# Performance work log

Hardware: AMD Instinct MI355X
Metric: run time of the kernel (lower is better)

Reference implementation:

```python
import jax, jax.numpy as jnp
import numpy as np

NEG_SLOPE = 0.01  # nn.LeakyReLU default


def setup_inputs() -> dict:
    key = jax.random.key(0)
    k1, k2, k3, k4, k5 = jax.random.split(key, 5)
    SLI, FEAT, NODE = 8, 64, 20000
    N = SLI * NODE          # 160000 graph nodes
    E = 2_560_000           # avg degree 16
    OUT = 64
    inputs = jax.random.normal(k1, (SLI, FEAT, NODE), dtype=jnp.float32)
    src = jax.random.randint(k2, (E,), 0, N, dtype=jnp.int64)
    dst = jax.random.randint(k3, (E,), 0, N, dtype=jnp.int64)
    # GraphConv params (glorot-ish scale)
    W = jax.random.normal(k4, (FEAT, OUT), dtype=jnp.float32) / np.sqrt(FEAT)
    b = jnp.zeros((OUT,), dtype=jnp.float32)
    return {"inputs": inputs, "W": W, "b": b, "src": src, "dst": dst}


def reference(inputs, W, b, src, dst):
    # inputs: [sli, feat, node] -> [sli*node, feat]  (dropout is eval-mode identity)
    sli, feat, node = inputs.shape
    x = jnp.transpose(inputs, (0, 2, 1)).reshape(-1, feat)
    N = sli * node
    ones = jnp.ones(src.shape, dtype=x.dtype)
    deg_out = jax.ops.segment_sum(ones, src, num_segments=N)  # out-degree of src
    deg_in = jax.ops.segment_sum(ones, dst, num_segments=N)   # in-degree of dst
    norm_src = jnp.where(deg_out > 0, deg_out, 1.0) ** -0.5
    norm_dst = jnp.where(deg_in > 0, deg_in, 1.0) ** -0.5
    # norm='both': scale src feats, sum-aggregate over edges, scale dst
    h = x * norm_src[:, None]
    agg = jax.ops.segment_sum(h[src], dst, num_segments=N)    # [N, feat]
    agg = agg * norm_dst[:, None]
    out = agg @ W + b                                          # [N, out]
    out = jax.nn.leaky_relu(out, NEG_SLOPE)
    # [N, out] -> [sli, node, out] -> [sli, out, node]
    return jnp.transpose(out.reshape(sli, node, -1), (0, 2, 1))
```

## Files before the change

### kernel.cpp

```cpp
#include <hip/hip_runtime.h>
#include <hip/hip_bf16.h>

constexpr int SLI  = 8;
constexpr int FEAT = 64;
constexpr int NODE = 20000;
constexpr int NTOT = SLI * NODE;
constexpr int OUTF = 64;
constexpr int CAP  = 48;
constexpr int NBD  = 625;
constexpr int NBS  = 313;
constexpr int BCAPD = 4864;
constexpr int BCAPS = 8960;
constexpr int EPB  = 4096;
constexpr int NDST = NTOT / 256;

typedef __attribute__((ext_vector_type(8))) short bf16x8;
typedef __attribute__((ext_vector_type(4))) float f32x4;

static __device__ inline unsigned short f2bf(float x) {
    unsigned u = __float_as_uint(x);
    unsigned r = (u + 0x7fffu + ((u >> 16) & 1u)) >> 16;
    return (unsigned short)r;
}

__global__ __launch_bounds__(256) void k_part(const int* __restrict__ src,
                                              const int* __restrict__ dst,
                                              int* __restrict__ cursor_d,
                                              unsigned* __restrict__ bucket_d,
                                              int* __restrict__ cursor_s,
                                              unsigned short* __restrict__ bucket_s, int E) {
    __shared__ unsigned       svalD[EPB];
    __shared__ unsigned short sbktD[EPB];
    __shared__ unsigned sS[EPB];
    __shared__ int histD[NBD], lcurD[NBD], baseD[NBD];
    __shared__ int histS[NBS], lcurS[NBS], baseS[NBS];
    __shared__ int goffD[64], goffS[64];
    int t  = threadIdx.x;
    int e0 = blockIdx.x * EPB;
    for (int i = t; i < NBD; i += 256) histD[i] = 0;
    for (int i = t; i < NBS; i += 256) histS[i] = 0;
    __syncthreads();
    int myS[16], myD[16];
#pragma unroll
    for (int i = 0; i < 4; ++i) {
        int j  = (e0 >> 2) + i * 256 + t;
        int b4 = j << 2;
        if (b4 + 3 < E) {
            int4 vs = ((const int4*)src)[j];
            int4 vd = ((const int4*)dst)[j];
            myS[4*i+0] = vs.x; myS[4*i+1] = vs.y; myS[4*i+2] = vs.z; myS[4*i+3] = vs.w;
            myD[4*i+0] = vd.x; myD[4*i+1] = vd.y; myD[4*i+2] = vd.z; myD[4*i+3] = vd.w;
        } else {
#pragma unroll
            for (int c = 0; c < 4; ++c) {
                int idx = b4 + c;
                myS[4*i+c] = (idx < E) ? src[idx] : -1;
                myD[4*i+c] = (idx < E) ? dst[idx] : -1;
            }
        }
    }
#pragma unroll
    for (int i = 0; i < 16; ++i) {
        if (myD[i] >= 0) {
            atomicAdd(&histD[myD[i] >> 8], 1);
            atomicAdd(&histS[myS[i] >> 9], 1);
        }
    }
    __syncthreads();
    int rbD[3], rbS[2];
#pragma unroll
    for (int i = 0; i < 3; ++i) {
        int bb = t + i * 256;
        rbD[i] = (bb < NBD) ? atomicAdd(&cursor_d[bb], histD[bb]) : 0;
    }
#pragma unroll
    for (int i = 0; i < 2; ++i) {
        int bb = t + i * 256;
        rbS[i] = (bb < NBS) ? atomicAdd(&cursor_s[bb], histS[bb]) : 0;
    }
    int wv = t >> 6, ln = t & 63;
    if (wv == 0) {
        int b0 = ln * 10, s = 0;
#pragma unroll
        for (int j = 0; j < 10; ++j) { int bb = b0 + j; if (bb < NBD) s += histD[bb]; }
        int x = s;
        for (int off = 1; off < 64; off <<= 1) {
            int y = __shfl_up(x, off, 64);
            if (ln >= off) x += y;
        }
        goffD[ln] = x - s;
    } else if (wv == 1) {
        int b0 = ln * 5, s = 0;
#pragma unroll
        for (int j = 0; j < 5; ++j) { int bb = b0 + j; if (bb < NBS) s += histS[bb]; }
        int x = s;
        for (int off = 1; off < 64; off <<= 1) {
            int y = __shfl_up(x, off, 64);
            if (ln >= off) x += y;
        }
        goffS[ln] = x - s;
    }
    asm volatile("s_waitcnt lgkmcnt(0)\n\ts_barrier" ::: "memory");
    for (int bb = t; bb < NBD; bb += 256) {
        int g = bb / 10;
        int sD = goffD[g];
        for (int k = g * 10; k < bb; ++k) sD += histD[k];
        lcurD[bb] = sD;
    }
    for (int bb = t; bb < NBS; bb += 256) {
        int g = bb / 5;
        int sS2 = goffS[g];
        for (int k = g * 5; k < bb; ++k) sS2 += histS[k];
        lcurS[bb] = sS2;
    }
    asm volatile("s_waitcnt lgkmcnt(0)\n\ts_barrier" ::: "memory");
#pragma unroll
    for (int i = 0; i < 16; ++i) {
        if (myD[i] >= 0) {
            int bD = myD[i] >> 8;
            int p  = atomicAdd(&lcurD[bD], 1);
            svalD[p] = ((unsigned)(myD[i] & 255) << 18) | (unsigned)myS[i];
            sbktD[p] = (unsigned short)bD;
            int bS = myS[i] >> 9;
            int q  = atomicAdd(&lcurS[bS], 1);
            sS[q] = ((unsigned)bS << 9) | (unsigned)(myS[i] & 511);
        }
    }
#pragma unroll
    for (int i = 0; i < 3; ++i) { int bb = t + i * 256; if (bb < NBD) baseD[bb] = rbD[i]; }
#pragma unroll
    for (int i = 0; i < 2; ++i) { int bb = t + i * 256; if (bb < NBS) baseS[bb] = rbS[i]; }
    __syncthreads();
    int nval = E - e0; if (nval > EPB) nval = EPB;
    for (int p = t; p < nval; p += 256) {
        int bD = sbktD[p];
        int wi = baseD[bD] + (p - (lcurD[bD] - histD[bD]));
        if (wi < BCAPD) bucket_d[(size_t)bD * BCAPD + wi] = svalD[p];
        unsigned vs = sS[p];
        int bS = vs >> 9;
        int wj = baseS[bS] + (p - (lcurS[bS] - histS[bS]));
        if (wj < BCAPS) bucket_s[(size_t)bS * BCAPS + wj] = (unsigned short)(vs & 511);
    }
}

__global__ __launch_bounds__(512) void k_fin(const int* __restrict__ cursor_d,
                                             const unsigned* __restrict__ bucket_d,
                                             const int* __restrict__ cursor_s,
                                             const unsigned short* __restrict__ bucket_s,
                                             int* __restrict__ col_ell,
                                             int* __restrict__ deg_in,
                                             int* __restrict__ deg_out) {
    __shared__ char lds[256 * CAP * 4 + 2048];
    int t = threadIdx.x;
    if (blockIdx.x < NDST) {
        int* ell = (int*)lds;
        int* cnt = (int*)(lds + 256 * CAP * 4);
        int b = blockIdx.x;
        if (t < 256) cnt[t] = 0;
        __syncthreads();
        int len = cursor_d[b]; if (len > BCAPD) len = BCAPD;
        const unsigned* p = bucket_d + (size_t)b * BCAPD;
        for (int i = t; i < len; i += 512) {
            unsigned e = p[i];
            int r = (e >> 18) & 255;
            int pos = atomicAdd(&cnt[r], 1);
            if (pos < CAP) ell[r * CAP + pos] = (int)(e & 0x3FFFFu);
        }
        __syncthreads();
        int node0 = b << 8;
        if (t < 256) deg_in[node0 + t] = cnt[t];
        size_t gbase = (size_t)node0 * CAP;
        const int4* lsrc = (const int4*)ell;
        int4* gdst = (int4*)(col_ell + gbase);
#pragma unroll
        for (int i = 0; i < 6; ++i)
            gdst[i * 512 + t] = lsrc[i * 512 + t];
    } else {
        int* cnt = (int*)lds;
        int b = blockIdx.x - NDST;
        cnt[t] = 0;
        __syncthreads();
        int len = cursor_s[b]; if (len > BCAPS) len = BCAPS;
        const unsigned short* p = bucket_s + (size_t)b * BCAPS;
        for (int i = t; i < len; i += 512)
            atomicAdd(&cnt[p[i]], 1);
        __syncthreads();
        int n0 = b << 9;
        if (n0 + t < NTOT) deg_out[n0 + t] = cnt[t];
    }
}

__global__ __launch_bounds__(256) void k_transpose(const float* __restrict__ in,
                                                   const int* __restrict__ deg_out,
                                                   unsigned short* __restrict__ xs) {
    __shared__ float tile[64][65];
    int sli = blockIdx.y;
    int n0  = blockIdx.x * 64;
    int t   = threadIdx.x;
    int fx  = t & 15;
    int fr  = t >> 4;
    const float* ip = in + (size_t)sli * FEAT * NODE;
    int nq = n0 + fx * 4;
#pragma unroll
    for (int i = 0; i < 4; ++i) {
        int f = fr + i * 16;
        float4 v = {0.f, 0.f, 0.f, 0.f};
        if (nq < NODE) v = *(const float4*)(ip + (size_t)f * NODE + nq);
        tile[f][fx * 4 + 0] = v.x;
        tile[f][fx * 4 + 1] = v.y;
        tile[f][fx * 4 + 2] = v.z;
        tile[f][fx * 4 + 3] = v.w;
    }
    __syncthreads();
    int h  = t & 31;
    int nr = t >> 5;
#pragma unroll
    for (int i = 0; i < 8; ++i) {
        int nl   = nr + i * 8;
        int node = n0 + nl;
        if (node < NODE) {
            int n = sli * NODE + node;
            int d = deg_out[n];
            float sc = rsqrtf(d > 0 ? (float)d : 1.f);
            unsigned lo = f2bf(tile[2 * h][nl] * sc);
            unsigned hi = f2bf(tile[2 * h + 1][nl] * sc);
            *(unsigned*)(xs + (size_t)n * 64 + 2 * h) = lo | (hi << 16);
        }
    }
}

__global__ __launch_bounds__(256) void k_agg_gemm(const int* __restrict__ deg_in,
                                                  const int* __restrict__ col_ell,
                                                  const unsigned short* __restrict__ xs,
                                                  const float* __restrict__ W,
                                                  const float* __restrict__ b,
                                                  float* __restrict__ out) {
    __shared__ char lds[18432];
    unsigned short* av = (unsigned short*)lds;
    unsigned short* wt = (unsigned short*)(lds + 9216);
    float (*otile)[65] = (float(*)[65])lds;

    int t    = threadIdx.x;
    int lane = t & 63;
    int w    = t >> 6;
    int g8   = lane >> 3;
    int f8   = lane & 7;
    int sli  = blockIdx.y;
    int n0   = blockIdx.x * 64;

#pragma unroll
    for (int i = 0; i < 16; ++i) {
        int idx = i * 256 + t;
        int f = idx >> 6, o = idx & 63;
        wt[o * 72 + f] = f2bf(W[idx]);
    }

    int m0 = w * 16;
    for (int ii = 0; ii < 16; ii += 2) {
        int rowA = m0 + ii, rowB = rowA + 1;
        int nodeA = n0 + rowA, nodeB = n0 + rowB;
        int nA = sli * NODE + nodeA, nB = sli * NODE + nodeB;
        int dA = (nodeA < NODE) ? deg_in[nA] : 0;
        int dB = (nodeB < NODE) ? deg_in[nB] : 0;
        int degA = dA < CAP ? dA : CAP;
        int degB = dB < CAP ? dB : CAP;
        int cA = (lane < degA) ? col_ell[(size_t)nA * CAP + lane] : NTOT;
        int cB = (lane < degB) ? col_ell[(size_t)nB * CAP + lane] : NTOT;
        float accA[8] = {0,0,0,0,0,0,0,0};
        float accB[8] = {0,0,0,0,0,0,0,0};
        int gmax = degA > degB ? degA : degB;
        int groups = (gmax + 7) >> 3;
#pragma unroll 2
        for (int j = 0; j < groups; ++j) {
            int idx = 8 * j + g8;
            int sA = __shfl(cA, idx, 64);
            int sB = __shfl(cB, idx, 64);
            uint4 vA = *(const uint4*)(xs + (size_t)sA * 64 + f8 * 8);
            uint4 vB = *(const uint4*)(xs + (size_t)sB * 64 + f8 * 8);
            accA[0] += __uint_as_float(vA.x << 16);
            accA[1] += __uint_as_float(vA.x & 0xffff0000u);
            accA[2] += __uint_as_float(vA.y << 16);
            accA[3] += __uint_as_float(vA.y & 0xffff0000u);
            accA[4] += __uint_as_float(vA.z << 16);
            accA[5] += __uint_as_float(vA.z & 0xffff0000u);
            accA[6] += __uint_as_float(vA.w << 16);
            accA[7] += __uint_as_float(vA.w & 0xffff0000u);
            accB[0] += __uint_as_float(vB.x << 16);
            accB[1] += __uint_as_float(vB.x & 0xffff0000u);
            accB[2] += __uint_as_float(vB.y << 16);
            accB[3] += __uint_as_float(vB.y & 0xffff0000u);
            accB[4] += __uint_as_float(vB.z << 16);
            accB[5] += __uint_as_float(vB.z & 0xffff0000u);
            accB[6] += __uint_as_float(vB.w << 16);
            accB[7] += __uint_as_float(vB.w & 0xffff0000u);
        }
#pragma unroll
        for (int k = 0; k < 8; ++k) {
            accA[k] += __shfl_xor(accA[k], 8, 64);
            accA[k] += __shfl_xor(accA[k], 16, 64);
            accA[k] += __shfl_xor(accA[k], 32, 64);
            accB[k] += __shfl_xor(accB[k], 8, 64);
            accB[k] += __shfl_xor(accB[k], 16, 64);
            accB[k] += __shfl_xor(accB[k], 32, 64);
        }
        if (g8 == 0) {
            float scA = rsqrtf(dA > 0 ? (float)dA : 1.f);
            float scB = rsqrtf(dB > 0 ? (float)dB : 1.f);
            uint4 hv;
            hv.x = (unsigned)f2bf(accA[0] * scA) | ((unsigned)f2bf(accA[1] * scA) << 16);
            hv.y = (unsigned)f2bf(accA[2] * scA) | ((unsigned)f2bf(accA[3] * scA) << 16);
            hv.z = (unsigned)f2bf(accA[4] * scA) | ((unsigned)f2bf(accA[5] * scA) << 16);
            hv.w = (unsigned)f2bf(accA[6] * scA) | ((unsigned)f2bf(accA[7] * scA) << 16);
            ((uint4*)(av + rowA * 72))[f8] = hv;
            hv.x = (unsigned)f2bf(accB[0] * scB) | ((unsigned)f2bf(accB[1] * scB) << 16);
            hv.y = (unsigned)f2bf(accB[2] * scB) | ((unsigned)f2bf(accB[3] * scB) << 16);
            hv.z = (unsigned)f2bf(accB[4] * scB) | ((unsigned)f2bf(accB[5] * scB) << 16);
            hv.w = (unsigned)f2bf(accB[6] * scB) | ((unsigned)f2bf(accB[7] * scB) << 16);
            ((uint4*)(av + rowB * 72))[f8] = hv;
        }
    }

    __syncthreads();

    int q = lane >> 4, r16 = lane & 15;
    bf16x8 afr[2], bfr[4][2];
#pragma unroll
    for (int ks = 0; ks < 2; ++ks)
        afr[ks] = *(const bf16x8*)(av + (m0 + r16) * 72 + ks * 32 + q * 8);
#pragma unroll
    for (int nt = 0; nt < 4; ++nt)
#pragma unroll
        for (int ks = 0; ks < 2; ++ks)
            bfr[nt][ks] = *(const bf16x8*)(wt + (nt * 16 + r16) * 72 + ks * 32 + q * 8);

    f32x4 acc4[4];
#pragma unroll
    for (int nt = 0; nt < 4; ++nt) acc4[nt] = (f32x4){0.f, 0.f, 0.f, 0.f};
#pragma unroll
    for (int nt = 0; nt < 4; ++nt)
#pragma unroll
        for (int ks = 0; ks < 2; ++ks)
            acc4[nt] = __builtin_amdgcn_mfma_f32_16x16x32_bf16(afr[ks], bfr[nt][ks], acc4[nt], 0, 0, 0);
    __syncthreads();

#pragma unroll
    for (int nt = 0; nt < 4; ++nt) {
        int oc = nt * 16 + r16;
        float bias = b[oc];
#pragma unroll
        for (int r = 0; r < 4; ++r) {
            float v = acc4[nt][r] + bias;
            v = v > 0.f ? v : 0.01f * v;
            otile[oc][m0 + q * 4 + r] = v;
        }
    }
    __syncthreads();

    const size_t obase = (size_t)sli * OUTF * NODE;
#pragma unroll
    for (int i = 0; i < 16; ++i) {
        int o    = w + i * 4;
        int node = n0 + lane;
        if (node < NODE)
            out[obase + (size_t)o * NODE + node] = otile[o][lane];
    }
}

extern "C" void kernel_launch(void* const* d_in, const int* in_sizes, int n_in,
                              void* d_out, int out_size, void* d_ws, size_t ws_size,
                              hipStream_t stream) {
    const float* inputs = (const float*)d_in[0];
    const float* W      = (const float*)d_in[1];
    const float* b      = (const float*)d_in[2];
    const int*   src    = (const int*)d_in[3];
    const int*   dst    = (const int*)d_in[4];
    float*       out    = (float*)d_out;
    const int E = in_sizes[3];

    char* ws = (char*)d_ws;
    int* deg_out = (int*)ws;
    int* deg_in  = (int*)(ws + (size_t)NTOT * 4);
    int* col_ell = (int*)(ws + (size_t)2 * NTOT * 4);
    char* R      = (char*)col_ell + (size_t)NTOT * CAP * 4;
    unsigned*       bucket_d = (unsigned*)R;
    unsigned short* bucket_s = (unsigned short*)(R + (size_t)NBD * BCAPD * 4);
    int*            cursors  = (int*)(R + (size_t)NBD * BCAPD * 4 + (size_t)NBS * BCAPS * 2);
    int* cursor_d = cursors;
    int* cursor_s = cursors + NBD;
    unsigned short* xs = (unsigned short*)R;

    hipMemsetAsync(cursors, 0, (size_t)(NBD + NBS) * 4, stream);
    hipMemsetAsync(xs + (size_t)NTOT * 64, 0, 64 * sizeof(unsigned short), stream);

    int PB = (E + EPB - 1) / EPB;
    k_part<<<PB, 256, 0, stream>>>(src, dst, cursor_d, bucket_d, cursor_s, bucket_s, E);

    k_fin<<<NDST + NBS, 512, 0, stream>>>(cursor_d, bucket_d, cursor_s, bucket_s,
                                          col_ell, deg_in, deg_out);

    dim3 tgrid((NODE + 63) / 64, SLI);
    k_transpose<<<tgrid, 256, 0, stream>>>(inputs, deg_out, xs);

    k_agg_gemm<<<tgrid, 256, 0, stream>>>(deg_in, col_ell, xs, W, b, out);
}
```

Measured before the change: 223.3 us.

## Fuse input transpose and out-degree scaling into the degree-count kernel

The source-degree blocks of k_fin now also transpose their 512 nodes of input, scale each node by rsqrt of its out-degree and write the bf16 xs rows. This removes the separate transpose kernel launch and the global deg_out round trip. To make it possible, the workspace layout gives xs its own region so it no longer aliases the buckets, with a fallback to the old path when the workspace is too small. k_part also moves from 256 to 512 threads per block with fewer edges per thread. The source-degree blocks are ordered first so their longer fused work starts early.

Measured after the change: 247.5 us. 10.8% more time.

```diff
diff --git a/kernel.cpp b/kernel.cpp
--- a/kernel.cpp
+++ b/kernel.cpp
@@ -23,7 +23,7 @@
     return (unsigned short)r;
 }
 
-__global__ __launch_bounds__(256) void k_part(const int* __restrict__ src,
+__global__ __launch_bounds__(512) void k_part(const int* __restrict__ src,
                                               const int* __restrict__ dst,
                                               int* __restrict__ cursor_d,
                                               unsigned* __restrict__ bucket_d,
@@ -37,13 +37,13 @@
     __shared__ int goffD[64], goffS[64];
     int t  = threadIdx.x;
     int e0 = blockIdx.x * EPB;
-    for (int i = t; i < NBD; i += 256) histD[i] = 0;
-    for (int i = t; i < NBS; i += 256) histS[i] = 0;
-    __syncthreads();
-    int myS[16], myD[16];
-#pragma unroll
-    for (int i = 0; i < 4; ++i) {
-        int j  = (e0 >> 2) + i * 256 + t;
+    for (int i = t; i < NBD; i += 512) histD[i] = 0;
+    for (int i = t; i < NBS; i += 512) histS[i] = 0;
+    __syncthreads();
+    int myS[8], myD[8];
+#pragma unroll
+    for (int i = 0; i < 2; ++i) {
+        int j  = (e0 >> 2) + i * 512 + t;
         int b4 = j << 2;
         if (b4 + 3 < E) {
             int4 vs = ((const int4*)src)[j];
@@ -60,24 +60,20 @@
         }
     }
 #pragma unroll
-    for (int i = 0; i < 16; ++i) {
+    for (int i = 0; i < 8; ++i) {
         if (myD[i] >= 0) {
             atomicAdd(&histD[myD[i] >> 8], 1);
             atomicAdd(&histS[myS[i] >> 9], 1);
         }
     }
     __syncthreads();
-    int rbD[3], rbS[2];
-#pragma unroll
-    for (int i = 0; i < 3; ++i) {
-        int bb = t + i * 256;
+    int rbD[2], rbS0;
+#pragma unroll
+    for (int i = 0; i < 2; ++i) {
+        int bb = t + i * 512;
         rbD[i] = (bb < NBD) ? atomicAdd(&cursor_d[bb], histD[bb]) : 0;
     }
-#pragma unroll
-    for (int i = 0; i < 2; ++i) {
-        int bb = t + i * 256;
-        rbS[i] = (bb < NBS) ? atomicAdd(&cursor_s[bb], histS[bb]) : 0;
-    }
+    rbS0 = (t < NBS) ? atomicAdd(&cursor_s[t], histS[t]) : 0;
     int wv = t >> 6, ln = t & 63;
     if (wv == 0) {
         int b0 = ln * 10, s = 0;
@@ -101,13 +97,13 @@
         goffS[ln] = x - s;
     }
     asm volatile("s_waitcnt lgkmcnt(0)\n\ts_barrier" ::: "memory");
-    for (int bb = t; bb < NBD; bb += 256) {
+    for (int bb = t; bb < NBD; bb += 512) {
         int g = bb / 10;
         int sD = goffD[g];
         for (int k = g * 10; k < bb; ++k) sD += histD[k];
         lcurD[bb] = sD;
     }
-    for (int bb = t; bb < NBS; bb += 256) {
+    for (int bb = t; bb < NBS; bb += 512) {
         int g = bb / 5;
         int sS2 = goffS[g];
         for (int k = g * 5; k < bb; ++k) sS2 += histS[k];
@@ -115,7 +111,7 @@
     }
     asm volatile("s_waitcnt lgkmcnt(0)\n\ts_barrier" ::: "memory");
 #pragma unroll
-    for (int i = 0; i < 16; ++i) {
+    for (int i = 0; i < 8; ++i) {
         if (myD[i] >= 0) {
             int bD = myD[i] >> 8;
             int p  = atomicAdd(&lcurD[bD], 1);
@@ -127,12 +123,11 @@
         }
     }
 #pragma unroll
-    for (int i = 0; i < 3; ++i) { int bb = t + i * 256; if (bb < NBD) baseD[bb] = rbD[i]; }
-#pragma unroll
-    for (int i = 0; i < 2; ++i) { int bb = t + i * 256; if (bb < NBS) baseS[bb] = rbS[i]; }
+    for (int i = 0; i < 2; ++i) { int bb = t + i * 512; if (bb < NBD) baseD[bb] = rbD[i]; }
+    if (t < NBS) baseS[t] = rbS0;
     __syncthreads();
     int nval = E - e0; if (nval > EPB) nval = EPB;
-    for (int p = t; p < nval; p += 256) {
+    for (int p = t; p < nval; p += 512) {
         int bD = sbktD[p];
         int wi = baseD[bD] + (p - (lcurD[bD] - histD[bD]));
         if (wi < BCAPD) bucket_d[(size_t)bD * BCAPD + wi] = svalD[p];
@@ -149,13 +144,83 @@
                                              const unsigned short* __restrict__ bucket_s,
                                              int* __restrict__ col_ell,
                                              int* __restrict__ deg_in,
-                                             int* __restrict__ deg_out) {
+                                             int* __restrict__ deg_out,
+                                             const float* __restrict__ in,
+                                             unsigned short* __restrict__ xs,
+                                             int fused) {
     __shared__ char lds[256 * CAP * 4 + 2048];
     int t = threadIdx.x;
-    if (blockIdx.x < NDST) {
+    if (blockIdx.x < NBS) {
+        int* cnt = (int*)lds;
+        int b = blockIdx.x;
+        cnt[t] = 0;
+        __syncthreads();
+        int len = cursor_s[b]; if (len > BCAPS) len = BCAPS;
+        const unsigned short* p = bucket_s + (size_t)b * BCAPS;
+        for (int i = t; i < len; i += 512)
+            atomicAdd(&cnt[p[i]], 1);
+        __syncthreads();
+        if (!fused) {
+            int n0 = b << 9;
+            if (n0 + t < NTOT) deg_out[n0 + t] = cnt[t];
+            return;
+        }
+        float (*tile)[65] = (float(*)[65])(lds + 2048);
+        for (int c = 0; c < 8; ++c) {
+            int gbase = (b << 9) + c * 64;
+            if (gbase >= NTOT) break;
+            int s0 = gbase / NODE;
+            bool uniform = (gbase + 63 < NTOT) && (s0 == (gbase + 63) / NODE);
+            if (uniform) {
+                int n0 = gbase - s0 * NODE;
+                const float* ip = in + (size_t)s0 * FEAT * NODE;
+                int fx = t & 15;
+                int fr = t >> 4;
+                int nq = n0 + fx * 4;
+#pragma unroll
+                for (int i = 0; i < 2; ++i) {
+                    int f = fr + i * 32;
+                    float4 v = *(const float4*)(ip + (size_t)f * NODE + nq);
+                    tile[f][fx * 4 + 0] = v.x;
+                    tile[f][fx * 4 + 1] = v.y;
+                    tile[f][fx * 4 + 2] = v.z;
+                    tile[f][fx * 4 + 3] = v.w;
+                }
+            } else {
+#pragma unroll
+                for (int i = 0; i < 8; ++i) {
+                    int idx = i * 512 + t;
+                    int nl = idx & 63, f = idx >> 6;
+                    int g = gbase + nl;
+                    float v = 0.f;
+                    if (g < NTOT) {
+                        int s = g / NODE, nd = g - s * NODE;
+                        v = in[(size_t)s * FEAT * NODE + (size_t)f * NODE + nd];
+                    }
+                    tile[f][nl] = v;
+                }
+            }
+            __syncthreads();
+            int h  = t & 31;
+            int nr = t >> 5;
+#pragma unroll
+            for (int i = 0; i < 4; ++i) {
+                int nl = nr + i * 16;
+                int g  = gbase + nl;
+                if (g < NTOT) {
+                    int d = cnt[c * 64 + nl];
+                    float sc = rsqrtf(d > 0 ? (float)d : 1.f);
+                    unsigned lo = f2bf(tile[2 * h][nl] * sc);
+                    unsigned hi = f2bf(tile[2 * h + 1][nl] * sc);
+                    *(unsigned*)(xs + (size_t)g * 64 + 2 * h) = lo | (hi << 16);
+                }
+            }
+            __syncthreads();
+        }
+    } else {
         int* ell = (int*)lds;
         int* cnt = (int*)(lds + 256 * CAP * 4);
-        int b = blockIdx.x;
+        int b = blockIdx.x - NBS;
         if (t < 256) cnt[t] = 0;
         __syncthreads();
         int len = cursor_d[b]; if (len > BCAPD) len = BCAPD;
@@ -175,18 +240,6 @@
 #pragma unroll
         for (int i = 0; i < 6; ++i)
             gdst[i * 512 + t] = lsrc[i * 512 + t];
-    } else {
-        int* cnt = (int*)lds;
-        int b = blockIdx.x - NDST;
-        cnt[t] = 0;
-        __syncthreads();
-        int len = cursor_s[b]; if (len > BCAPS) len = BCAPS;
-        const unsigned short* p = bucket_s + (size_t)b * BCAPS;
-        for (int i = t; i < len; i += 512)
-            atomicAdd(&cnt[p[i]], 1);
-        __syncthreads();
-        int n0 = b << 9;
-        if (n0 + t < NTOT) deg_out[n0 + t] = cnt[t];
     }
 }
 
@@ -378,28 +431,53 @@
     const int E = in_sizes[3];
 
     char* ws = (char*)d_ws;
-    int* deg_out = (int*)ws;
-    int* deg_in  = (int*)(ws + (size_t)NTOT * 4);
-    int* col_ell = (int*)(ws + (size_t)2 * NTOT * 4);
-    char* R      = (char*)col_ell + (size_t)NTOT * CAP * 4;
-    unsigned*       bucket_d = (unsigned*)R;
-    unsigned short* bucket_s = (unsigned short*)(R + (size_t)NBD * BCAPD * 4);
-    int*            cursors  = (int*)(R + (size_t)NBD * BCAPD * 4 + (size_t)NBS * BCAPS * 2);
-    int* cursor_d = cursors;
-    int* cursor_s = cursors + NBD;
-    unsigned short* xs = (unsigned short*)R;
-
-    hipMemsetAsync(cursors, 0, (size_t)(NBD + NBS) * 4, stream);
-    hipMemsetAsync(xs + (size_t)NTOT * 64, 0, 64 * sizeof(unsigned short), stream);
+    const size_t szDegIn = (size_t)NTOT * 4;
+    const size_t szEll   = (size_t)NTOT * CAP * 4;
+    const size_t szBd    = (size_t)NBD * BCAPD * 4;
+    const size_t szBs    = (size_t)NBS * BCAPS * 2;
+    const size_t szCur   = (size_t)(NBD + NBS) * 4;
+    const size_t szXs    = (size_t)(NTOT + 1) * 64 * 2;
+    const size_t needA   = szDegIn + szEll + szBd + szBs + szCur + szXs;
 
     int PB = (E + EPB - 1) / EPB;
-    k_part<<<PB, 256, 0, stream>>>(src, dst, cursor_d, bucket_d, cursor_s, bucket_s, E);
-
-    k_fin<<<NDST + NBS, 512, 0, stream>>>(cursor_d, bucket_d, cursor_s, bucket_s,
-                                          col_ell, deg_in, deg_out);
-
     dim3 tgrid((NODE + 63) / 64, SLI);
-    k_transpose<<<tgrid, 256, 0, stream>>>(inputs, deg_out, xs);
-
-    k_agg_gemm<<<tgrid, 256, 0, stream>>>(deg_in, col_ell, xs, W, b, out);
-}
+
+    if (ws_size >= needA) {
+        int* deg_in  = (int*)ws;
+        int* col_ell = (int*)(ws + szDegIn);
+        unsigned*       bucket_d = (unsigned*)(ws + szDegIn + szEll);
+        unsigned short* bucket_s = (unsigned short*)(ws + szDegIn + szEll + szBd);
+        int*            cursors  = (int*)(ws + szDegIn + szEll + szBd + szBs);
+        int* cursor_d = cursors;
+        int* cursor_s = cursors + NBD;
+        unsigned short* xs = (unsigned short*)(ws + szDegIn + szEll + szBd + szBs + szCur);
+
+        hipMemsetAsync(cursors, 0, szCur, stream);
+        hipMemsetAsync(xs + (size_t)NTOT * 64, 0, 64 * sizeof(unsigned short), stream);
+
+        k_part<<<PB, 512, 0, stream>>>(src, dst, cursor_d, bucket_d, cursor_s, bucket_s, E);
+        k_fin<<<NBS + NDST, 512, 0, stream>>>(cursor_d, bucket_d, cursor_s, bucket_s,
+                                              col_ell, deg_in, nullptr, inputs, xs, 1);
+        k_agg_gemm<<<tgrid, 256, 0, stream>>>(deg_in, col_ell, xs, W, b, out);
+    } else {
+        int* deg_out = (int*)ws;
+        int* deg_in  = (int*)(ws + szDegIn);
+        int* col_ell = (int*)(ws + 2 * szDegIn);
+        char* R      = ws + 2 * szDegIn + szEll;
+        unsigned*       bucket_d = (unsigned*)R;
+        unsigned short* bucket_s = (unsigned short*)(R + szBd);
+        int*            cursors  = (int*)(R + szBd + szBs);
+        int* cursor_d = cursors;
+        int* cursor_s = cursors + NBD;
+        unsigned short* xs = (unsigned short*)R;
+
+        hipMemsetAsync(cursors, 0, szCur, stream);
+        hipMemsetAsync(xs + (size_t)NTOT * 64, 0, 64 * sizeof(unsigned short), stream);
+
+        k_part<<<PB, 512, 0, stream>>>(src, dst, cursor_d, bucket_d, cursor_s, bucket_s, E);
+        k_fin<<<NBS + NDST, 512, 0, stream>>>(cursor_d, bucket_d, cursor_s, bucket_s,
+                                              col_ell, deg_in, deg_out, inputs, xs, 0);
+        k_transpose<<<tgrid, 256, 0, stream>>>(inputs, deg_out, xs);
+        k_agg_gemm<<<tgrid, 256, 0, stream>>>(deg_in, col_ell, xs, W, b, out);
+    }
+}
```
